# Optimization experiments

Measured on AMD Instinct MI355X. Metric: run time of the kernel, lower is better.

The kernel has to match this reference:

```python
import jax, jax.numpy as jnp
import numpy as np

# Constants derived from quantiles=[0.1..0.9] (deciles), df = 9.
QUANTILES = jnp.array([0.1, 0.2, 0.3, 0.4, 0.5, 0.6, 0.7, 0.8, 0.9], dtype=jnp.float32)
# scipy.stats.norm.ppf(quantiles), cast to float32 as in the torch module
Z_SCORES = jnp.array([-1.2815516, -0.8416212, -0.5244005, -0.2533471, 0.0,
                      0.2533471, 0.5244005, 0.8416212, 1.2815516], dtype=jnp.float32)
# expected bin probabilities: q0, diffs, 1-q_last -> all 0.1 for deciles
EXPECTED_PCT = jnp.full((10,), 0.1, dtype=jnp.float32)
# chi2.ppf(1 - p, df=9) for p in QUANTILES (precomputed with scipy offline)
CRIT = jnp.array([14.683657, 12.242145, 10.656372, 9.413640, 8.342832,
                  7.357034, 6.393306, 5.380053, 4.168159], dtype=jnp.float32)
MAX_CRIT = 14.683657
SHARPNESS = 100.0  # sigmoid steepness for the soft histogram


def setup_inputs() -> dict:
    key = jax.random.key(0)
    x = jax.random.normal(key, (16777216,), dtype=jnp.float32)
    return {"x": x}


def reference(x):
    n = x.shape[0]
    mean = x.mean()
    std = jnp.std(x, ddof=1)  # torch.std uses Bessel's correction
    z = (x - mean) / std  # [n]
    # soft cumulative counts at each quantile threshold: [K]
    cum = jax.nn.sigmoid(SHARPNESS * (Z_SCORES[:, None] - z[None, :])).sum(axis=1)
    # bin counts: first cum, consecutive diffs, remainder n - last cum -> [K+1]
    actual = jnp.concatenate([cum[:1], jnp.diff(cum),
                              jnp.asarray(n, z.dtype)[None] - cum[-1:]])
    expected = n * EXPECTED_PCT
    chi2_stat = jnp.sum((actual - expected) ** 2 / (expected + 1e-7))
    # differentiable interpolation of p-value
    w = jax.nn.softmax(-jnp.abs(chi2_stat - CRIT))
    p_value_estimate = 1.0 - jnp.sum(w * QUANTILES)
    excess = jax.nn.relu((chi2_stat - MAX_CRIT) / 100.0)
    return p_value_estimate + excess
```

## Files before the change

### kernel.cpp

```cpp
#include <hip/hip_runtime.h>
#include <math.h>


#if __has_builtin(__builtin_amdgcn_exp2f)
#define EXP2F(x) __builtin_amdgcn_exp2f(x)
#else
#define EXP2F(x) exp2f(x)
#endif
#if __has_builtin(__builtin_amdgcn_rcpf)
#define RCPF(x) __builtin_amdgcn_rcpf(x)
#else
#define RCPF(x) (1.0f / (x))
#endif

#define NBLK 1024

static __device__ __forceinline__ double wave_reduce_d(double v) {
#pragma unroll
    for (int off = 32; off > 0; off >>= 1) v += __shfl_down(v, off);
    return v;
}

__device__ __constant__ double d_ZS[9] = {
    -1.2815516, -0.8416212, -0.5244005, -0.2533471, 0.0,
    0.2533471,  0.5244005,  0.8416212,  1.2815516};

__device__ void epilogue(const double* cum, float* out, int n) {
    const double CRIT[9] = {14.683657, 12.242145, 10.656372, 9.413640, 8.342832,
                            7.357034,  6.393306,  5.380053,  4.168159};
    const double nd = (double)n;
    double actual[10];
    actual[0] = cum[0];
#pragma unroll
    for (int k = 1; k < 9; ++k) actual[k] = cum[k] - cum[k - 1];
    actual[9] = nd - cum[8];
    const double expected = nd * (double)0.1f;
    const double denom = expected + 1e-7;
    double chi2 = 0.0;
#pragma unroll
    for (int j = 0; j < 10; ++j) {
        double d = actual[j] - expected;
        chi2 += d * d / denom;
    }
    double dneg[9], m = -1e300;
#pragma unroll
    for (int k = 0; k < 9; ++k) {
        dneg[k] = -fabs(chi2 - CRIT[k]);
        if (dneg[k] > m) m = dneg[k];
    }
    double W = 0.0, PQ = 0.0;
#pragma unroll
    for (int k = 0; k < 9; ++k) {
        double w = exp(dneg[k] - m);
        W += w;
        PQ += w * (0.1 * (double)(k + 1));
    }
    double p = 1.0 - PQ / W;
    double excess = (chi2 - 14.683657) / 100.0;
    if (excess < 0.0) excess = 0.0;
    out[0] = (float)(p + excess);
}

__global__ __launch_bounds__(256) void pass1_stats(const float* __restrict__ x,
                                                   double* __restrict__ part1, int n) {
    const int tx = threadIdx.x;
    const int tid = blockIdx.x * 256 + tx;
    const int nthreads = NBLK * 256;
    const int n4 = n >> 2;
    const float4* __restrict__ x4 = (const float4*)x;

    float fs = 0.f, fss = 0.f;
    for (int i = tid; i < n4; i += nthreads) {
        float4 v = x4[i];
        fs += (v.x + v.y) + (v.z + v.w);
        fss = fmaf(v.x, v.x, fss); fss = fmaf(v.y, v.y, fss);
        fss = fmaf(v.z, v.z, fss); fss = fmaf(v.w, v.w, fss);
    }
    if (blockIdx.x == 0 && tx == 0) {
        for (int j = n4 << 2; j < n; ++j) {
            float v = x[j];
            fs += v;
            fss = fmaf(v, v, fss);
        }
    }
    double s = wave_reduce_d((double)fs);
    double ss = wave_reduce_d((double)fss);
    __shared__ double sm[4][2];
    const int lane = tx & 63, wid = tx >> 6;
    if (lane == 0) { sm[wid][0] = s; sm[wid][1] = ss; }
    __syncthreads();
    if (tx == 0) {
        part1[2 * blockIdx.x] = (sm[0][0] + sm[1][0]) + (sm[2][0] + sm[3][0]);
        part1[2 * blockIdx.x + 1] = (sm[0][1] + sm[1][1]) + (sm[2][1] + sm[3][1]);
    }
}

__global__ __launch_bounds__(256) void pass2_cum(const float* __restrict__ x,
                                                 const double* __restrict__ part1,
                                                 double* __restrict__ part2, int n) {
    const int tx = threadIdx.x;
    const int lane = tx & 63, wid = tx >> 6;

    __shared__ double sm[4][9];
    __shared__ float sConst[11];
    {
        double s = 0.0, ss = 0.0;
        for (int b = tx; b < NBLK; b += 256) {
            s += part1[2 * b];
            ss += part1[2 * b + 1];
        }
        double rs = wave_reduce_d(s);
        double rss = wave_reduce_d(ss);
        if (lane == 0) { sm[wid][0] = rs; sm[wid][1] = rss; }
        __syncthreads();
        if (tx == 0) {
            double ts = (sm[0][0] + sm[1][0]) + (sm[2][0] + sm[3][0]);
            double tss = (sm[0][1] + sm[1][1]) + (sm[2][1] + sm[3][1]);
            const double Ld = 144.26950408889634;
            const double nd = (double)n;
            const double mean = ts / nd;
            const double var = (tss - ts * ts / nd) / (nd - 1.0);
            const double inv_std = 1.0 / sqrt(var);
            sConst[0] = (float)(0.5 * Ld * inv_std);
            sConst[1] = (float)(-0.5 * Ld * inv_std * mean);
#pragma unroll
            for (int k = 0; k < 9; ++k)
                sConst[2 + k] = (float)exp2(-0.5 * Ld * d_ZS[k]);
        }
        __syncthreads();
    }
    const float S2 = sConst[0], B2 = sConst[1];
    float sg[9];
#pragma unroll
    for (int k = 0; k < 9; ++k) sg[k] = sConst[2 + k];

    float acc[9];
#pragma unroll
    for (int k = 0; k < 9; ++k) acc[k] = 0.f;

    auto process = [&](float xv) {
        const float E = EXP2F(fmaf(xv, S2, B2));
#pragma unroll
        for (int k = 0; k < 9; ++k) {
            const float t = E * sg[k];
            acc[k] += RCPF(1.0f + t * t);
        }
    };

    const int tid = blockIdx.x * 256 + tx;
    const int nthreads = NBLK * 256;
    const int n4 = n >> 2;
    const float4* __restrict__ x4 = (const float4*)x;

    for (int i = tid; i < n4; i += nthreads) {
        float4 v = x4[i];
        process(v.x); process(v.y); process(v.z); process(v.w);
    }
    if (blockIdx.x == 0 && tx == 0) {
        for (int jj = n4 << 2; jj < n; ++jj) process(x[jj]);
    }

    __syncthreads();
#pragma unroll
    for (int k = 0; k < 9; ++k) {
        double r = wave_reduce_d((double)acc[k]);
        if (lane == 0) sm[wid][k] = r;
    }
    __syncthreads();
    if (tx < 9) {
        part2[9 * blockIdx.x + tx] = (sm[0][tx] + sm[1][tx]) + (sm[2][tx] + sm[3][tx]);
    }
}

__global__ __launch_bounds__(256) void finalize_kernel(const double* __restrict__ part2,
                                                       float* __restrict__ out, int n) {
    const int tx = threadIdx.x;
    double acc[9];
#pragma unroll
    for (int k = 0; k < 9; ++k) acc[k] = 0.0;
    for (int b = tx; b < NBLK; b += 256) {
#pragma unroll
        for (int k = 0; k < 9; ++k) acc[k] += part2[9 * b + k];
    }
    __shared__ double sm[4][9];
    const int lane = tx & 63, wid = tx >> 6;
#pragma unroll
    for (int k = 0; k < 9; ++k) {
        double r = wave_reduce_d(acc[k]);
        if (lane == 0) sm[wid][k] = r;
    }
    __syncthreads();
    if (tx == 0) {
        double cum[9];
#pragma unroll
        for (int k = 0; k < 9; ++k)
            cum[k] = (sm[0][k] + sm[1][k]) + (sm[2][k] + sm[3][k]);
        epilogue(cum, out, n);
    }
}

extern "C" void kernel_launch(void* const* d_in, const int* in_sizes, int n_in,
                              void* d_out, int out_size, void* d_ws, size_t ws_size,
                              hipStream_t stream) {
    const float* x = (const float*)d_in[0];
    const int n = in_sizes[0];
    double* part1 = (double*)d_ws;
    double* part2 = part1 + 2 * NBLK;

    pass1_stats<<<NBLK, 256, 0, stream>>>(x, part1, n);
    pass2_cum<<<NBLK, 256, 0, stream>>>(x, part1, part2, n);
    finalize_kernel<<<1, 256, 0, stream>>>(part2, (float*)d_out, n);
}
```

Measured before the change: 125.0 us.

## Stream input through double-buffered async global-to-LDS loads with fewer blocks

Both passes now use a fixed decomposition when n matches exactly: 256 blocks, each wave owning a contiguous 4096-float4 slice. Each wave streams its slice through a per-wave double buffer in LDS using async global_load_lds, issuing the next chunk before processing the current one. The aim is to keep memory requests in flight while the ALU work runs, and to cut block and partial-reduction overhead. In exchange, occupancy drops to one 256-thread block per CU with 64KB of LDS per block, which may leave the compute-heavy sigmoid pass with too little latency hiding. A generic fallback path is kept for other sizes.

```diff
diff --git a/kernel.cpp b/kernel.cpp
--- a/kernel.cpp
+++ b/kernel.cpp
@@ -13,7 +13,16 @@
 #define RCPF(x) (1.0f / (x))
 #endif
 
-#define NBLK 1024
+#define NBLK 256
+#define WAITCNT_VM0 0x0f70
+
+typedef const __attribute__((address_space(1))) unsigned int* gas1_u32p;
+typedef __attribute__((address_space(3))) unsigned int* las3_u32p;
+
+static __device__ __forceinline__ void async_load16(const float4* g, float4* l) {
+    __builtin_amdgcn_global_load_lds((gas1_u32p)(const void*)g,
+                                     (las3_u32p)(void*)l, 16, 0, 0);
+}
 
 static __device__ __forceinline__ double wave_reduce_d(double v) {
 #pragma unroll
@@ -61,32 +70,61 @@
     out[0] = (float)(p + excess);
 }
 
+
 __global__ __launch_bounds__(256) void pass1_stats(const float* __restrict__ x,
                                                    double* __restrict__ part1, int n) {
     const int tx = threadIdx.x;
-    const int tid = blockIdx.x * 256 + tx;
-    const int nthreads = NBLK * 256;
+    const int lane = tx & 63, wid = tx >> 6;
     const int n4 = n >> 2;
     const float4* __restrict__ x4 = (const float4*)x;
+    __shared__ float4 stage[4][2][512];
 
     float fs = 0.f, fss = 0.f;
-    for (int i = tid; i < n4; i += nthreads) {
-        float4 v = x4[i];
-        fs += (v.x + v.y) + (v.z + v.w);
-        fss = fmaf(v.x, v.x, fss); fss = fmaf(v.y, v.y, fss);
-        fss = fmaf(v.z, v.z, fss); fss = fmaf(v.w, v.w, fss);
-    }
-    if (blockIdx.x == 0 && tx == 0) {
-        for (int j = n4 << 2; j < n; ++j) {
-            float v = x[j];
-            fs += v;
-            fss = fmaf(v, v, fss);
-        }
-    }
+
+    if (n4 == NBLK * 256 * 64 && (n & 3) == 0) {
+        const float4* wbase = x4 + blockIdx.x * 16384 + wid * 4096;
+        float4* sbuf0 = &stage[wid][0][0];
+        float4* sbuf1 = &stage[wid][1][0];
+#pragma unroll
+        for (int r = 0; r < 8; ++r) async_load16(wbase + r * 64 + lane, sbuf0 + r * 64);
+        for (int u = 0; u < 8; ++u) {
+            float4* cur = (u & 1) ? sbuf1 : sbuf0;
+            float4* nxt = (u & 1) ? sbuf0 : sbuf1;
+            __builtin_amdgcn_s_waitcnt(WAITCNT_VM0);
+            if (u < 7) {
+                const float4* gb = wbase + (u + 1) * 512;
+#pragma unroll
+                for (int r = 0; r < 8; ++r) async_load16(gb + r * 64 + lane, nxt + r * 64);
+            }
+#pragma unroll
+            for (int r = 0; r < 8; ++r) {
+                float4 v = cur[r * 64 + lane];
+                fs += (v.x + v.y) + (v.z + v.w);
+                fss = fmaf(v.x, v.x, fss); fss = fmaf(v.y, v.y, fss);
+                fss = fmaf(v.z, v.z, fss); fss = fmaf(v.w, v.w, fss);
+            }
+        }
+    } else {
+        const int tid = blockIdx.x * 256 + tx;
+        const int nthreads = NBLK * 256;
+        for (int i = tid; i < n4; i += nthreads) {
+            float4 v = x4[i];
+            fs += (v.x + v.y) + (v.z + v.w);
+            fss = fmaf(v.x, v.x, fss); fss = fmaf(v.y, v.y, fss);
+            fss = fmaf(v.z, v.z, fss); fss = fmaf(v.w, v.w, fss);
+        }
+        if (blockIdx.x == 0 && tx == 0) {
+            for (int j = n4 << 2; j < n; ++j) {
+                float v = x[j];
+                fs += v;
+                fss = fmaf(v, v, fss);
+            }
+        }
+    }
+
     double s = wave_reduce_d((double)fs);
     double ss = wave_reduce_d((double)fss);
     __shared__ double sm[4][2];
-    const int lane = tx & 63, wid = tx >> 6;
     if (lane == 0) { sm[wid][0] = s; sm[wid][1] = ss; }
     __syncthreads();
     if (tx == 0) {
@@ -100,9 +138,10 @@
                                                  double* __restrict__ part2, int n) {
     const int tx = threadIdx.x;
     const int lane = tx & 63, wid = tx >> 6;
-
+    __shared__ float4 stage[4][2][512];
     __shared__ double sm[4][9];
     __shared__ float sConst[11];
+
     {
         double s = 0.0, ss = 0.0;
         for (int b = tx; b < NBLK; b += 256) {
@@ -147,17 +186,40 @@
         }
     };
 
-    const int tid = blockIdx.x * 256 + tx;
-    const int nthreads = NBLK * 256;
     const int n4 = n >> 2;
     const float4* __restrict__ x4 = (const float4*)x;
 
-    for (int i = tid; i < n4; i += nthreads) {
-        float4 v = x4[i];
-        process(v.x); process(v.y); process(v.z); process(v.w);
-    }
-    if (blockIdx.x == 0 && tx == 0) {
-        for (int jj = n4 << 2; jj < n; ++jj) process(x[jj]);
+    if (n4 == NBLK * 256 * 64 && (n & 3) == 0) {
+        const float4* wbase = x4 + blockIdx.x * 16384 + wid * 4096;
+        float4* sbuf0 = &stage[wid][0][0];
+        float4* sbuf1 = &stage[wid][1][0];
+#pragma unroll
+        for (int r = 0; r < 8; ++r) async_load16(wbase + r * 64 + lane, sbuf0 + r * 64);
+        for (int u = 0; u < 8; ++u) {
+            float4* cur = (u & 1) ? sbuf1 : sbuf0;
+            float4* nxt = (u & 1) ? sbuf0 : sbuf1;
+            __builtin_amdgcn_s_waitcnt(WAITCNT_VM0);
+            if (u < 7) {
+                const float4* gb = wbase + (u + 1) * 512;
+#pragma unroll
+                for (int r = 0; r < 8; ++r) async_load16(gb + r * 64 + lane, nxt + r * 64);
+            }
+#pragma unroll
+            for (int r = 0; r < 8; ++r) {
+                float4 v = cur[r * 64 + lane];
+                process(v.x); process(v.y); process(v.z); process(v.w);
+            }
+        }
+    } else {
+        const int tid = blockIdx.x * 256 + tx;
+        const int nthreads = NBLK * 256;
+        for (int i = tid; i < n4; i += nthreads) {
+            float4 v = x4[i];
+            process(v.x); process(v.y); process(v.z); process(v.w);
+        }
+        if (blockIdx.x == 0 && tx == 0) {
+            for (int jj = n4 << 2; jj < n; ++jj) process(x[jj]);
+        }
     }
 
     __syncthreads();
```

New measurement: 125.5 us. No clear change (+0.4%).
